# Performance work log

Hardware: AMD Instinct MI355X
Metric: run time of the kernel (lower is better)

Reference implementation:

```python
import jax, jax.numpy as jnp
import numpy as np

N, MAX_SIZE, SPATIAL = 50000, 32, 27
CH_IN, CH_OUT = 128, 128


def setup_inputs() -> dict:
    key = jax.random.key(0)
    k1, k2, k3, k4 = jax.random.split(key, 4)
    feat_in = jax.random.normal(k1, (N, CH_IN), dtype=jnp.float32)
    select_mat = jax.random.uniform(k2, (N, MAX_SIZE, SPATIAL), dtype=jnp.float32)
    # kaiming-uniform-ish init for weight of shape [SPATIAL, CH_OUT*CH_IN]
    fan_in = CH_OUT * CH_IN
    bound = np.sqrt(6.0 / fan_in)
    weight = jax.random.uniform(k3, (SPATIAL, CH_OUT * CH_IN), dtype=jnp.float32,
                                minval=-bound, maxval=bound)
    neighbor_idx = jax.random.randint(k4, (N, MAX_SIZE), 0, N, dtype=jnp.int64)
    return {"feat_in": feat_in, "select_mat": select_mat,
            "weight": weight, "neighbor_idx": neighbor_idx}


def reference(feat_in, select_mat, weight, neighbor_idx):
    # feat_in: [N, I]; select_mat: [N, M, S]; weight: [S, O*I]; neighbor_idx: [N, M]
    ch_in = feat_in.shape[1]
    spatial = weight.shape[0]
    ch_out = weight.shape[1] // ch_in
    w = weight.reshape(spatial, ch_out, ch_in)          # [S, O, I]
    patch_feat = feat_in[neighbor_idx]                  # irregular gather -> [N, M, I]
    # Original math: out[n,o] = sum_m sum_s sel[n,m,s] * W[s,o,i] * pf[n,m,i]
    # Contract neighbor dim first to avoid the [N, M, O, I] intermediate.
    t = jnp.einsum('nms,nmi->nsi', select_mat, patch_feat)   # [N, S, I]
    feat_out = jnp.einsum('nsi,soi->no', t, w)               # [N, O]
    return feat_out[:, :, None]                              # [N, O, 1]
```

## Files before the change

### kernel.cpp

```cpp
#include <hip/hip_runtime.h>


#define N_CHI 128
#define N_SP  27
#define N_M   32
#define KDIM  (N_SP * N_CHI)
#define SEL_STRIDE (N_M * N_SP)

typedef short s16x8 __attribute__((ext_vector_type(8)));
typedef s16x8 __attribute__((may_alias)) s16x8_a;
typedef unsigned short u16x8 __attribute__((ext_vector_type(8)));
typedef u16x8 __attribute__((may_alias)) u16x8_a;
typedef unsigned int u32x2 __attribute__((ext_vector_type(2)));
typedef u32x2 __attribute__((may_alias)) u32x2_a;
typedef float f32x4 __attribute__((ext_vector_type(4)));
typedef float f32x16 __attribute__((ext_vector_type(16)));

typedef __attribute__((address_space(3))) unsigned int as3_u32;
typedef __attribute__((address_space(1))) const unsigned int as1_u32;

static __device__ __forceinline__ unsigned short f2bf(float f) {
  unsigned int u = __float_as_uint(f);
  u += 0x7FFFu + ((u >> 16) & 1u);
  return (unsigned short)(u >> 16);
}

__global__ __launch_bounds__(128) void wconv_kernel(const float* __restrict__ w,
                                                    unsigned short* __restrict__ Wt) {
  const int s = blockIdx.x;
  const int o = blockIdx.y;
  const int i = threadIdx.x;
  Wt[((size_t)o * N_SP + s) * N_CHI + i] = f2bf(w[((size_t)s * 128 + o) * N_CHI + i]);
}

__global__ __launch_bounds__(256) void phase1_kernel(
    const float* __restrict__ feat, const float* __restrict__ sel,
    const int* __restrict__ nidx, unsigned short* __restrict__ T,
    int nbase, int nend) {
  __shared__ __align__(16) unsigned short selT[4][32 * 40];
  __shared__ __align__(16) unsigned short tbuf[4][N_SP * 128];
  const int wave = threadIdx.x >> 6;
  const int lane = threadIdx.x & 63;
  const int n = nbase + (int)blockIdx.x * 4 + wave;
  if (n >= nend) return;
  unsigned short* st = selT[wave];
  unsigned short* tb = tbuf[wave];

  const float* selp = sel + (size_t)n * SEL_STRIDE;
#pragma unroll
  for (int it = 0; it < 16; ++it) {
    int e = it * 64 + lane;
    int m = e >> 5, s = e & 31;
    float v = (s < N_SP) ? selp[m * N_SP + s] : 0.0f;
    st[s * 40 + m] = f2bf(v);
  }

  const int q = lane >> 5;
  const int col = lane & 31;

  const int* ip = nidx + (size_t)n * N_M;
  int rows[16];
#pragma unroll
  for (int ks = 0; ks < 2; ++ks)
#pragma unroll
    for (int j = 0; j < 8; ++j) rows[ks * 8 + j] = ip[ks * 16 + q * 8 + j];

  const s16x8 bf0 = *(const s16x8_a*)&st[col * 40 + q * 8];
  const s16x8 bf1 = *(const s16x8_a*)&st[col * 40 + 16 + q * 8];

#pragma unroll
  for (int ti = 0; ti < 4; ++ti) {
    const int icol = ti * 32 + col;
    float fv[16];
#pragma unroll
    for (int t = 0; t < 16; ++t) fv[t] = feat[(size_t)rows[t] * N_CHI + icol];
    s16x8 af0, af1;
#pragma unroll
    for (int j = 0; j < 8; ++j) {
      af0[j] = (short)f2bf(fv[j]);
      af1[j] = (short)f2bf(fv[8 + j]);
    }
    f32x16 acc = {0.f, 0.f, 0.f, 0.f, 0.f, 0.f, 0.f, 0.f,
                  0.f, 0.f, 0.f, 0.f, 0.f, 0.f, 0.f, 0.f};
    acc = __builtin_amdgcn_mfma_f32_32x32x16_bf16(af0, bf0, acc, 0, 0, 0);
    acc = __builtin_amdgcn_mfma_f32_32x32x16_bf16(af1, bf1, acc, 0, 0, 0);
    if (col < N_SP) {
#pragma unroll
      for (int g = 0; g < 4; ++g) {
        const int sub = ti * 8 + g * 2 + q;
        const int phys = col * 128 + (((sub ^ ((col & 7) << 2))) << 2);
        u32x2 pk;
        pk[0] = (unsigned int)f2bf(acc[4 * g + 0]) | ((unsigned int)f2bf(acc[4 * g + 1]) << 16);
        pk[1] = (unsigned int)f2bf(acc[4 * g + 2]) | ((unsigned int)f2bf(acc[4 * g + 3]) << 16);
        *(u32x2_a*)&tb[phys] = pk;
      }
    }
  }

  unsigned short* Tn = T + (size_t)(n - nbase) * KDIM;
#pragma unroll
  for (int it = 0; it < 7; ++it) {
    const int P = it * 64 + lane;
    if (P < 432) {
      const int c = P >> 4;
      const int sub = (P << 1) & 31;
      const int phys = c * 128 + (((sub ^ ((c & 7) << 2))) << 2);
      *(u16x8_a*)&Tn[(size_t)P * 8] = *(const u16x8_a*)&tb[phys];
    }
  }
}

__global__ __launch_bounds__(256) void phase2_kernel(
    const unsigned short* __restrict__ T, const unsigned short* __restrict__ Wt,
    float* __restrict__ out, int nbase, int N) {
  __shared__ __align__(16) unsigned short Alds[128 * 64];
  __shared__ __align__(16) unsigned short Blds[128 * 64];
  const int tid = threadIdx.x;
  const int lane = tid & 63;
  const int wbase = tid & ~63;
  const int wave = tid >> 6;
  const int wm = wave & 1, wn = wave >> 1;
  const int quad = lane >> 4, l16 = lane & 15;
  const size_t rowbase = (size_t)blockIdx.x * 128;

  f32x4 acc[4][4];
#pragma unroll
  for (int a = 0; a < 4; ++a)
#pragma unroll
    for (int b = 0; b < 4; ++b) acc[a][b] = (f32x4){0.f, 0.f, 0.f, 0.f};

  const unsigned short* aga[4];
  const unsigned short* bga[4];
#pragma unroll
  for (int it = 0; it < 4; ++it) {
    const int slot = it * 256 + tid;
    const int r = slot >> 3, bp = slot & 7;
    aga[it] = T + (rowbase + r) * KDIM + ((bp ^ (r & 7)) << 3);
    bga[it] = Wt + (size_t)r * KDIM + ((bp ^ (r & 7)) << 3);
  }

  for (int kt = 0; kt < KDIM / 64; ++kt) {
    const int k0 = kt * 64;
#pragma unroll
    for (int it = 0; it < 4; ++it) {
      __builtin_amdgcn_global_load_lds(
          (as1_u32*)(const void*)(aga[it] + k0),
          (as3_u32*)(void*)&Alds[(it * 256 + wbase) * 8], 16, 0, 0);
      __builtin_amdgcn_global_load_lds(
          (as1_u32*)(const void*)(bga[it] + k0),
          (as3_u32*)(void*)&Blds[(it * 256 + wbase) * 8], 16, 0, 0);
    }
    __syncthreads();
#pragma unroll
    for (int ks = 0; ks < 2; ++ks) {
      const int bg = ks * 4 + quad;
      s16x8 af[4], bfr[4];
#pragma unroll
      for (int mt = 0; mt < 4; ++mt) {
        const int m = wm * 64 + mt * 16 + l16;
        af[mt] = *(const s16x8_a*)&Alds[m * 64 + ((bg ^ (m & 7)) << 3)];
      }
#pragma unroll
      for (int nt = 0; nt < 4; ++nt) {
        const int o = wn * 64 + nt * 16 + l16;
        bfr[nt] = *(const s16x8_a*)&Blds[o * 64 + ((bg ^ (o & 7)) << 3)];
      }
#pragma unroll
      for (int mt = 0; mt < 4; ++mt)
#pragma unroll
        for (int nt = 0; nt < 4; ++nt)
          acc[mt][nt] = __builtin_amdgcn_mfma_f32_16x16x32_bf16(af[mt], bfr[nt],
                                                                acc[mt][nt], 0, 0, 0);
    }
    __syncthreads();
  }

#pragma unroll
  for (int mt = 0; mt < 4; ++mt) {
    const int growb = nbase + (int)rowbase + wm * 64 + mt * 16 + quad * 4;
#pragma unroll
    for (int r = 0; r < 4; ++r) {
      const int grow = growb + r;
      if (grow < N) {
#pragma unroll
        for (int nt = 0; nt < 4; ++nt) {
          const int o = wn * 64 + nt * 16 + l16;
          out[(size_t)grow * 128 + o] = acc[mt][nt][r];
        }
      }
    }
  }
}

extern "C" void kernel_launch(void* const* d_in, const int* in_sizes, int n_in,
                              void* d_out, int out_size, void* d_ws, size_t ws_size,
                              hipStream_t stream) {
  const float* feat = (const float*)d_in[0];
  const float* sel  = (const float*)d_in[1];
  const float* wgt  = (const float*)d_in[2];
  const int*   nidx = (const int*)d_in[3];
  float* out = (float*)d_out;
  const int N = in_sizes[0] / N_CHI;

  unsigned short* Wt = (unsigned short*)d_ws;
  const size_t WT_ELEMS = (size_t)128 * KDIM;
  unsigned short* T = Wt + WT_ELEMS;

  wconv_kernel<<<dim3(N_SP, 128), 128, 0, stream>>>(wgt, Wt);

  const size_t bytes_for_T = (ws_size > WT_ELEMS * 2) ? (ws_size - WT_ELEMS * 2) : 0;
  long cap_rows = (long)(bytes_for_T / ((size_t)KDIM * 2));
  long NC = (cap_rows / 128) * 128;
  const long Nfull = (((long)N + 127) / 128) * 128;
  if (NC > Nfull) NC = Nfull;
  if (NC <= 0) return;

  for (long nb = 0; nb < N; nb += NC) {
    long rows = (long)N - nb;
    if (rows > NC) rows = NC;
    const long rows128 = ((rows + 127) / 128) * 128;
    phase1_kernel<<<dim3((unsigned)((rows + 3) / 4)), 256, 0, stream>>>(
        feat, sel, nidx, T, (int)nb, (int)(nb + rows));
    phase2_kernel<<<dim3((unsigned)(rows128 / 128)), 256, 0, stream>>>(
        T, Wt, out, (int)nb, N);
  }
}
```

Measured before the change: 545.7 us.

## Pre-convert features to bf16 and retile phase-2 GEMM to 64-row, 128-K tiles

A new kernel converts feat_in to bf16 once, so the phase-1 neighbour gather reads half the bytes and skips per-element conversion. The phase-1 LDS swizzle is changed to a 16-granule XOR. Phase 2 now uses 64-row M tiles with a 128-wide K step, which doubles the block count for better CU occupancy and halves the number of K iterations. The cost is an extra conversion pass, more workspace, a larger B tile per block (Wt is reloaded by twice as many blocks), and fewer MFMAs per B load.

Measured after the change: 556.1 us. Within noise of the previous version (+1.9%).

```diff
diff --git a/kernel.cpp b/kernel.cpp
--- a/kernel.cpp
+++ b/kernel.cpp
@@ -11,9 +11,12 @@
 typedef s16x8 __attribute__((may_alias)) s16x8_a;
 typedef unsigned short u16x8 __attribute__((ext_vector_type(8)));
 typedef u16x8 __attribute__((may_alias)) u16x8_a;
+typedef unsigned short u16x4 __attribute__((ext_vector_type(4)));
+typedef u16x4 __attribute__((may_alias)) u16x4_a;
 typedef unsigned int u32x2 __attribute__((ext_vector_type(2)));
 typedef u32x2 __attribute__((may_alias)) u32x2_a;
 typedef float f32x4 __attribute__((ext_vector_type(4)));
+typedef f32x4 __attribute__((may_alias)) f32x4_a;
 typedef float f32x16 __attribute__((ext_vector_type(16)));
 
 typedef __attribute__((address_space(3))) unsigned int as3_u32;
@@ -33,8 +36,20 @@
   Wt[((size_t)o * N_SP + s) * N_CHI + i] = f2bf(w[((size_t)s * 128 + o) * N_CHI + i]);
 }
 
+__global__ __launch_bounds__(256) void featconv_kernel(
+    const float* __restrict__ feat, unsigned short* __restrict__ featb, int total4) {
+  const int t = blockIdx.x * 256 + threadIdx.x;
+  if (t < total4) {
+    f32x4 v = ((const f32x4_a*)feat)[t];
+    u16x4 o;
+#pragma unroll
+    for (int j = 0; j < 4; ++j) o[j] = f2bf(v[j]);
+    ((u16x4_a*)featb)[t] = o;
+  }
+}
+
 __global__ __launch_bounds__(256) void phase1_kernel(
-    const float* __restrict__ feat, const float* __restrict__ sel,
+    const unsigned short* __restrict__ featb, const float* __restrict__ sel,
     const int* __restrict__ nidx, unsigned short* __restrict__ T,
     int nbase, int nend) {
   __shared__ __align__(16) unsigned short selT[4][32 * 40];
@@ -59,11 +74,12 @@
   const int col = lane & 31;
 
   const int* ip = nidx + (size_t)n * N_M;
-  int rows[16];
+  size_t roff[16];
 #pragma unroll
   for (int ks = 0; ks < 2; ++ks)
 #pragma unroll
-    for (int j = 0; j < 8; ++j) rows[ks * 8 + j] = ip[ks * 16 + q * 8 + j];
+    for (int j = 0; j < 8; ++j)
+      roff[ks * 8 + j] = (size_t)ip[ks * 16 + q * 8 + j] << 7;
 
   const s16x8 bf0 = *(const s16x8_a*)&st[col * 40 + q * 8];
   const s16x8 bf1 = *(const s16x8_a*)&st[col * 40 + 16 + q * 8];
@@ -71,14 +87,14 @@
 #pragma unroll
   for (int ti = 0; ti < 4; ++ti) {
     const int icol = ti * 32 + col;
-    float fv[16];
-#pragma unroll
-    for (int t = 0; t < 16; ++t) fv[t] = feat[(size_t)rows[t] * N_CHI + icol];
+    unsigned short fv[16];
+#pragma unroll
+    for (int t = 0; t < 16; ++t) fv[t] = featb[roff[t] + icol];
     s16x8 af0, af1;
 #pragma unroll
     for (int j = 0; j < 8; ++j) {
-      af0[j] = (short)f2bf(fv[j]);
-      af1[j] = (short)f2bf(fv[8 + j]);
+      af0[j] = (short)fv[j];
+      af1[j] = (short)fv[8 + j];
     }
     f32x16 acc = {0.f, 0.f, 0.f, 0.f, 0.f, 0.f, 0.f, 0.f,
                   0.f, 0.f, 0.f, 0.f, 0.f, 0.f, 0.f, 0.f};
@@ -87,12 +103,12 @@
     if (col < N_SP) {
 #pragma unroll
       for (int g = 0; g < 4; ++g) {
-        const int sub = ti * 8 + g * 2 + q;
-        const int phys = col * 128 + (((sub ^ ((col & 7) << 2))) << 2);
+        const int b16 = ti * 4 + g;
+        const int phys16 = b16 ^ (col & 15);
         u32x2 pk;
         pk[0] = (unsigned int)f2bf(acc[4 * g + 0]) | ((unsigned int)f2bf(acc[4 * g + 1]) << 16);
         pk[1] = (unsigned int)f2bf(acc[4 * g + 2]) | ((unsigned int)f2bf(acc[4 * g + 3]) << 16);
-        *(u32x2_a*)&tb[phys] = pk;
+        *(u32x2_a*)&tb[col * 128 + phys16 * 8 + q * 4] = pk;
       }
     }
   }
@@ -103,9 +119,9 @@
     const int P = it * 64 + lane;
     if (P < 432) {
       const int c = P >> 4;
-      const int sub = (P << 1) & 31;
-      const int phys = c * 128 + (((sub ^ ((c & 7) << 2))) << 2);
-      *(u16x8_a*)&Tn[(size_t)P * 8] = *(const u16x8_a*)&tb[phys];
+      const int b16 = P & 15;
+      const int phys16 = b16 ^ (c & 15);
+      *(u16x8_a*)&Tn[(size_t)P * 8] = *(const u16x8_a*)&tb[c * 128 + phys16 * 8];
     }
   }
 }
@@ -113,60 +129,66 @@
 __global__ __launch_bounds__(256) void phase2_kernel(
     const unsigned short* __restrict__ T, const unsigned short* __restrict__ Wt,
     float* __restrict__ out, int nbase, int N) {
-  __shared__ __align__(16) unsigned short Alds[128 * 64];
-  __shared__ __align__(16) unsigned short Blds[128 * 64];
+  __shared__ __align__(16) unsigned short Alds[64 * 128];
+  __shared__ __align__(16) unsigned short Blds[128 * 128];
   const int tid = threadIdx.x;
   const int lane = tid & 63;
   const int wbase = tid & ~63;
   const int wave = tid >> 6;
   const int wm = wave & 1, wn = wave >> 1;
   const int quad = lane >> 4, l16 = lane & 15;
-  const size_t rowbase = (size_t)blockIdx.x * 128;
-
-  f32x4 acc[4][4];
-#pragma unroll
-  for (int a = 0; a < 4; ++a)
+  const size_t rowbase = (size_t)blockIdx.x * 64;
+
+  f32x4 acc[2][4];
+#pragma unroll
+  for (int a = 0; a < 2; ++a)
 #pragma unroll
     for (int b = 0; b < 4; ++b) acc[a][b] = (f32x4){0.f, 0.f, 0.f, 0.f};
 
   const unsigned short* aga[4];
-  const unsigned short* bga[4];
+  const unsigned short* bga[8];
 #pragma unroll
   for (int it = 0; it < 4; ++it) {
     const int slot = it * 256 + tid;
-    const int r = slot >> 3, bp = slot & 7;
-    aga[it] = T + (rowbase + r) * KDIM + ((bp ^ (r & 7)) << 3);
-    bga[it] = Wt + (size_t)r * KDIM + ((bp ^ (r & 7)) << 3);
-  }
-
-  for (int kt = 0; kt < KDIM / 64; ++kt) {
-    const int k0 = kt * 64;
-#pragma unroll
-    for (int it = 0; it < 4; ++it) {
+    const int r = slot >> 4, bp = slot & 15;
+    aga[it] = T + (rowbase + r) * KDIM + ((bp ^ (r & 15)) << 3);
+  }
+#pragma unroll
+  for (int it = 0; it < 8; ++it) {
+    const int slot = it * 256 + tid;
+    const int r = slot >> 4, bp = slot & 15;
+    bga[it] = Wt + (size_t)r * KDIM + ((bp ^ (r & 15)) << 3);
+  }
+
+  for (int kt = 0; kt < KDIM / 128; ++kt) {
+    const int k0 = kt * 128;
+#pragma unroll
+    for (int it = 0; it < 4; ++it)
       __builtin_amdgcn_global_load_lds(
           (as1_u32*)(const void*)(aga[it] + k0),
           (as3_u32*)(void*)&Alds[(it * 256 + wbase) * 8], 16, 0, 0);
+#pragma unroll
+    for (int it = 0; it < 8; ++it)
       __builtin_amdgcn_global_load_lds(
           (as1_u32*)(const void*)(bga[it] + k0),
           (as3_u32*)(void*)&Blds[(it * 256 + wbase) * 8], 16, 0, 0);
-    }
     __syncthreads();
 #pragma unroll
-    for (int ks = 0; ks < 2; ++ks) {
+    for (int ks = 0; ks < 4; ++ks) {
       const int bg = ks * 4 + quad;
-      s16x8 af[4], bfr[4];
-#pragma unroll
-      for (int mt = 0; mt < 4; ++mt) {
-        const int m = wm * 64 + mt * 16 + l16;
-        af[mt] = *(const s16x8_a*)&Alds[m * 64 + ((bg ^ (m & 7)) << 3)];
+      s16x8 af[2], bfr[4];
+#pragma unroll
+      for (int mt = 0; mt < 2; ++mt) {
+        const int m = wm * 32 + mt * 16 + l16;
+        af[mt] = *(const s16x8_a*)&Alds[m * 128 + ((bg ^ (m & 15)) << 3)];
       }
 #pragma unroll
       for (int nt = 0; nt < 4; ++nt) {
         const int o = wn * 64 + nt * 16 + l16;
-        bfr[nt] = *(const s16x8_a*)&Blds[o * 64 + ((bg ^ (o & 7)) << 3)];
-      }
-#pragma unroll
-      for (int mt = 0; mt < 4; ++mt)
+        bfr[nt] = *(const s16x8_a*)&Blds[o * 128 + ((bg ^ (o & 15)) << 3)];
+      }
+#pragma unroll
+      for (int mt = 0; mt < 2; ++mt)
 #pragma unroll
         for (int nt = 0; nt < 4; ++nt)
           acc[mt][nt] = __builtin_amdgcn_mfma_f32_16x16x32_bf16(af[mt], bfr[nt],
@@ -176,8 +198,8 @@
   }
 
 #pragma unroll
-  for (int mt = 0; mt < 4; ++mt) {
-    const int growb = nbase + (int)rowbase + wm * 64 + mt * 16 + quad * 4;
+  for (int mt = 0; mt < 2; ++mt) {
+    const int growb = nbase + (int)rowbase + wm * 32 + mt * 16 + quad * 4;
 #pragma unroll
     for (int r = 0; r < 4; ++r) {
       const int grow = growb + r;
@@ -201,27 +223,33 @@
   const int*   nidx = (const int*)d_in[3];
   float* out = (float*)d_out;
   const int N = in_sizes[0] / N_CHI;
+  const int total = in_sizes[0];
 
   unsigned short* Wt = (unsigned short*)d_ws;
   const size_t WT_ELEMS = (size_t)128 * KDIM;
-  unsigned short* T = Wt + WT_ELEMS;
+  unsigned short* featb = Wt + WT_ELEMS;
+  const size_t FB_ELEMS = (size_t)N * N_CHI;
+  unsigned short* T = featb + FB_ELEMS;
 
   wconv_kernel<<<dim3(N_SP, 128), 128, 0, stream>>>(wgt, Wt);
-
-  const size_t bytes_for_T = (ws_size > WT_ELEMS * 2) ? (ws_size - WT_ELEMS * 2) : 0;
+  featconv_kernel<<<dim3((unsigned)((total / 4 + 255) / 256)), 256, 0, stream>>>(
+      feat, featb, total / 4);
+
+  const size_t head = (WT_ELEMS + FB_ELEMS) * 2;
+  const size_t bytes_for_T = (ws_size > head) ? (ws_size - head) : 0;
   long cap_rows = (long)(bytes_for_T / ((size_t)KDIM * 2));
-  long NC = (cap_rows / 128) * 128;
-  const long Nfull = (((long)N + 127) / 128) * 128;
+  long NC = (cap_rows / 64) * 64;
+  const long Nfull = (((long)N + 63) / 64) * 64;
   if (NC > Nfull) NC = Nfull;
   if (NC <= 0) return;
 
   for (long nb = 0; nb < N; nb += NC) {
     long rows = (long)N - nb;
     if (rows > NC) rows = NC;
-    const long rows128 = ((rows + 127) / 128) * 128;
+    const long rows64 = ((rows + 63) / 64) * 64;
     phase1_kernel<<<dim3((unsigned)((rows + 3) / 4)), 256, 0, stream>>>(
-        feat, sel, nidx, T, (int)nb, (int)(nb + rows));
-    phase2_kernel<<<dim3((unsigned)(rows128 / 128)), 256, 0, stream>>>(
+        featb, sel, nidx, T, (int)nb, (int)(nb + rows));
+    phase2_kernel<<<dim3((unsigned)(rows64 / 64)), 256, 0, stream>>>(
         T, Wt, out, (int)nb, N);
   }
 }
```
